# Optimization experiments

Measured on AMD Instinct MI355X. Metric: run time of the kernel, lower is better.

Reference implementation:

```python
import jax, jax.numpy as jnp
import numpy as np

B, C, H, W = 64, 3, 256, 256
K = 2  # multi_n_num
EPS_NORM = 1e-8
EPS_DEN = 1e-7
SCALE = 0.01


def setup_inputs() -> dict:
    key = jax.random.key(0)
    ka, kp, kn, kj = jax.random.split(key, 4)
    a = jax.random.normal(ka, (B, C, H, W), dtype=jnp.float32)
    p = jax.random.normal(kp, (B, C, H, W), dtype=jnp.float32)
    n = jax.random.normal(kn, (B, C, H, W), dtype=jnp.float32)
    # sample_with_j(B, 2, i) -> [i, random j != i]
    ar = jnp.arange(B, dtype=jnp.int64)
    off = jax.random.randint(kj, (B,), 1, B)  # offset in [1, B) guarantees j != i
    neg_idx = jnp.stack([ar, (ar + off) % B], axis=1).astype(jnp.int64)  # [B, K]
    return {"a": a, "p": p, "n": n, "neg_idx": neg_idx}


def _fft_norm(x):
    # torch.fft.fft2 over last two dims -> complex, same rank as x
    f = jnp.fft.fft2(x, axes=(-2, -1))  # [B, C, H, W] complex64
    # torch.norm(f, p=2, dim=1, keepdim=True) on complex = sqrt(sum |f|^2 over C)
    nrm = jnp.sqrt(jnp.sum(jnp.abs(f) ** 2, axis=1, keepdims=True))
    return f / (nrm + EPS_NORM) * SCALE


def reference(a, p, n, neg_idx):
    af = _fft_norm(a)
    pf = _fft_norm(p)
    nf = _fft_norm(n)
    # L1Loss on complex tensors = mean |diff| (complex magnitude)
    d_ap = jnp.mean(jnp.abs(af - pf), axis=(1, 2, 3))  # [B]
    n_sel = nf[neg_idx]  # [B, K, C, H, W]
    d_an = jnp.mean(jnp.abs(af[:, None] - n_sel), axis=(2, 3, 4))  # [B, K]
    contrastive = jnp.sum(d_ap[:, None] / (d_an + EPS_DEN))
    return contrastive / (K * B)
```

## Files before the change

### kernel.cpp

```cpp
#include <hip/hip_runtime.h>
#include <hip/hip_fp16.h>

#define B_ 64
#define SW_ 132
#define SIMG_ (256 * SW_)
#define TIMG_ (3 * SIMG_)
#define TELEMS_ ((size_t)B_ * TIMG_)
#define SST_ 257

__device__ __forceinline__ float2 cmul(float2 a, float2 b) {
  return make_float2(a.x * b.x - a.y * b.y, a.x * b.y + a.y * b.x);
}
__device__ __forceinline__ unsigned f2u(float2 v) {
  __half2 h = __float22half2_rn(v);
  return __builtin_bit_cast(unsigned, h);
}
__device__ __forceinline__ float2 u2f(unsigned u) {
  return __half22float2(__builtin_bit_cast(__half2, u));
}

__device__ __forceinline__ void bfly4(float2 x[4], float2 ta, float2 tb, float2 tc, bool tw) {
  float2 a = make_float2(x[0].x + x[2].x, x[0].y + x[2].y);
  float2 b = make_float2(x[0].x - x[2].x, x[0].y - x[2].y);
  float2 c = make_float2(x[1].x + x[3].x, x[1].y + x[3].y);
  float2 d = make_float2(x[1].x - x[3].x, x[1].y - x[3].y);
  float2 y1 = make_float2(b.x + d.y, b.y - d.x);
  float2 y2 = make_float2(a.x - c.x, a.y - c.y);
  float2 y3 = make_float2(b.x - d.y, b.y + d.x);
  x[0] = make_float2(a.x + c.x, a.y + c.y);
  if (tw) { y1 = cmul(y1, ta); y2 = cmul(y2, tb); y3 = cmul(y3, tc); }
  x[1] = y1; x[2] = y2; x[3] = y3;
}

__device__ __forceinline__ void swap16(unsigned& A, unsigned& B) {
  asm("v_permlane16_swap_b32 %0, %1" : "+v"(A), "+v"(B));
}
__device__ __forceinline__ void swap32(unsigned& A, unsigned& B) {
  asm("v_permlane32_swap_b32 %0, %1" : "+v"(A), "+v"(B));
}

template <int BIT>
__device__ __forceinline__ void xsel(unsigned& A, unsigned& B, int r) {
  bool hi = (r >> BIT) & 1;
  int send = hi ? (int)A : (int)B;
  int got;
  if constexpr (BIT == 0)
    got = __builtin_amdgcn_update_dpp(0, send, 0xB1, 0xF, 0xF, false);
  else if constexpr (BIT == 1)
    got = __builtin_amdgcn_update_dpp(0, send, 0x4E, 0xF, 0xF, false);
  else if constexpr (BIT == 2)
    got = __builtin_amdgcn_ds_swizzle(send, 0x101F);
  else
    got = __builtin_amdgcn_ds_swizzle(send, 0x201F);
  if (hi) A = (unsigned)got; else B = (unsigned)got;
}

__device__ __forceinline__ void xdig45(unsigned u[4]) {
  swap16(u[0], u[1]);
  swap16(u[2], u[3]);
  swap32(u[0], u[2]);
  swap32(u[1], u[3]);
}
template <int BIT>
__device__ __forceinline__ void xdig(unsigned u[4], int r) {
  xsel<BIT>(u[0], u[1], r);
  xsel<BIT>(u[2], u[3], r);
  xsel<BIT + 1>(u[0], u[2], r);
  xsel<BIT + 1>(u[1], u[3], r);
}

template <int NF>
__device__ __forceinline__ void fft256(float2 (&x)[NF][4], unsigned (&u)[NF][4],
                                       int r, const float2 tw[9]) {
#pragma unroll
  for (int f = 0; f < NF; ++f) bfly4(x[f], tw[0], tw[1], tw[2], true);
#pragma unroll
  for (int f = 0; f < NF; ++f)
#pragma unroll
    for (int s = 0; s < 4; ++s) u[f][s] = f2u(x[f][s]);
#pragma unroll
  for (int f = 0; f < NF; ++f) xdig45(u[f]);
#pragma unroll
  for (int f = 0; f < NF; ++f)
#pragma unroll
    for (int s = 0; s < 4; ++s) x[f][s] = u2f(u[f][s]);
#pragma unroll
  for (int f = 0; f < NF; ++f) bfly4(x[f], tw[3], tw[4], tw[5], true);
#pragma unroll
  for (int f = 0; f < NF; ++f)
#pragma unroll
    for (int s = 0; s < 4; ++s) u[f][s] = f2u(x[f][s]);
#pragma unroll
  for (int f = 0; f < NF; ++f) xdig<2>(u[f], r);
#pragma unroll
  for (int f = 0; f < NF; ++f)
#pragma unroll
    for (int s = 0; s < 4; ++s) x[f][s] = u2f(u[f][s]);
#pragma unroll
  for (int f = 0; f < NF; ++f) bfly4(x[f], tw[6], tw[7], tw[8], true);
#pragma unroll
  for (int f = 0; f < NF; ++f)
#pragma unroll
    for (int s = 0; s < 4; ++s) u[f][s] = f2u(x[f][s]);
#pragma unroll
  for (int f = 0; f < NF; ++f) xdig<0>(u[f], r);
#pragma unroll
  for (int f = 0; f < NF; ++f)
#pragma unroll
    for (int s = 0; s < 4; ++s) x[f][s] = u2f(u[f][s]);
#pragma unroll
  for (int f = 0; f < NF; ++f) bfly4(x[f], tw[0], tw[0], tw[0], false);
#pragma unroll
  for (int f = 0; f < NF; ++f)
#pragma unroll
    for (int s = 0; s < 4; ++s) u[f][s] = f2u(x[f][s]);
}

__global__ __launch_bounds__(1024, 4) void fft2_fused(const float* __restrict__ a,
                                                      const float* __restrict__ p,
                                                      const float* __restrict__ n,
                                                      unsigned* __restrict__ outbase) {
  __shared__ unsigned S[129 * SST_];

  int tid = threadIdx.x;
  int wv = tid >> 6;
  int r = tid & 63;
  int tensor = blockIdx.x / 192;
  int plane = blockIdx.x % 192;
  const float* in = (tensor == 0 ? a : (tensor == 1 ? p : n)) + (size_t)plane * 65536;
  unsigned* outp = outbase + (size_t)tensor * TELEMS_ + (size_t)plane * SIMG_;

  float2 tw[9];
  {
    float s, c;
    __sincosf(-6.283185307179586f * (float)r / 256.0f, &s, &c);
    tw[0] = make_float2(c, s); tw[1] = cmul(tw[0], tw[0]); tw[2] = cmul(tw[1], tw[0]);
    __sincosf(-6.283185307179586f * (float)(r & 15) / 64.0f, &s, &c);
    tw[3] = make_float2(c, s); tw[4] = cmul(tw[3], tw[3]); tw[5] = cmul(tw[4], tw[3]);
    __sincosf(-6.283185307179586f * (float)(r & 3) / 16.0f, &s, &c);
    tw[6] = make_float2(c, s); tw[7] = cmul(tw[6], tw[6]); tw[8] = cmul(tw[7], tw[6]);
  }
  int m = ((r & 3) << 4) | (((r >> 2) & 3) << 2) | (r >> 4);
  int mp = (64 - m) & 63;
  int rp = ((mp >> 4) & 3) | (((mp >> 2) & 3) << 2) | ((mp & 3) << 4);

  for (int it = 0; it < 2; ++it) {
    float2 x[4][4]; unsigned u[4][4];
#pragma unroll
    for (int f = 0; f < 4; ++f) {
      int q = it * 64 + wv + 16 * f;
      const float* rw = in + (size_t)(2 * q) * 256;
#pragma unroll
      for (int j = 0; j < 4; ++j)
        x[f][j] = make_float2(rw[r + 64 * j], rw[256 + r + 64 * j]);
    }
    fft256<4>(x, u, r, tw);
#pragma unroll
    for (int f = 0; f < 4; ++f) {
      int q = it * 64 + wv + 16 * f;
      unsigned m0 = (unsigned)__shfl((int)u[f][0], rp, 64);
      unsigned m2 = (unsigned)__shfl((int)u[f][2], rp, 64);
      unsigned m3 = (unsigned)__shfl((int)u[f][3], rp, 64);
      float2 Zk0 = u2f(u[f][0]);
      float2 Zk1 = u2f(u[f][1]);
      float2 Zm0 = u2f((m == 0) ? m0 : m3);
      float2 Zm1 = u2f((m == 0) ? m3 : m2);
      float2 Aa = make_float2(0.5f * (Zk0.x + Zm0.x), 0.5f * (Zk0.y - Zm0.y));
      float2 Ab = make_float2(0.5f * (Zk0.y + Zm0.y), 0.5f * (Zm0.x - Zk0.x));
      float2 Ba = make_float2(0.5f * (Zk1.x + Zm1.x), 0.5f * (Zk1.y - Zm1.y));
      float2 Bb = make_float2(0.5f * (Zk1.y + Zm1.y), 0.5f * (Zm1.x - Zk1.x));
      S[m * SST_ + 2 * q]          = f2u(Aa);
      S[m * SST_ + 2 * q + 1]      = f2u(Ab);
      S[(64 + m) * SST_ + 2 * q]     = f2u(Ba);
      S[(64 + m) * SST_ + 2 * q + 1] = f2u(Bb);
      if (r == 0) {
        float2 Z = u2f(u[f][2]);
        S[128 * SST_ + 2 * q]     = f2u(make_float2(Z.x, 0.0f));
        S[128 * SST_ + 2 * q + 1] = f2u(make_float2(Z.y, 0.0f));
      }
    }
  }

  __syncthreads();

  for (int it = 0; it < 2; ++it) {
    float2 x[4][4]; unsigned u[4][4];
#pragma unroll
    for (int f = 0; f < 4; ++f) {
      const unsigned* row = S + (size_t)(it * 64 + wv + 16 * f) * SST_;
#pragma unroll
      for (int j = 0; j < 4; ++j) x[f][j] = u2f(row[r + 64 * j]);
    }
    fft256<4>(x, u, r, tw);
#pragma unroll
    for (int f = 0; f < 4; ++f) {
      int c = it * 64 + wv + 16 * f;
      *(uint4*)(outp + (size_t)c * 256 + 4 * r) =
          make_uint4(u[f][0], u[f][1], u[f][2], u[f][3]);
    }
  }
  if (wv == 0) {
    float2 x1[1][4]; unsigned u1[1][4];
    const unsigned* srow = S + 128 * SST_;
#pragma unroll
    for (int j = 0; j < 4; ++j) x1[0][j] = u2f(srow[r + 64 * j]);
    fft256<1>(x1, u1, r, tw);
    *(uint4*)(outp + (size_t)128 * 256 + 4 * r) =
        make_uint4(u1[0][0], u1[0][1], u1[0][2], u1[0][3]);
  }
  if (wv >= 13) {
    int c = 129 + (wv - 13);
    *(uint4*)(outp + (size_t)c * 256 + 4 * r) = make_uint4(0, 0, 0, 0);
  }
}

__device__ __forceinline__ float cab2(float2 v) { return v.x * v.x + v.y * v.y; }

__global__ __launch_bounds__(256) void dist_kernel(const unsigned* __restrict__ af,
                                                   const unsigned* __restrict__ pf,
                                                   const unsigned* __restrict__ nf,
                                                   const int* __restrict__ neg,
                                                   float* __restrict__ acc) {
  int b = blockIdx.y;
  int j = (neg[1] == 0) ? (int)((const long long*)neg)[b * 2 + 1] : neg[b * 2 + 1];
  size_t ab = (size_t)b * TIMG_;
  size_t jb = (size_t)j * TIMG_;
  int t4 = blockIdx.x * 256 + threadIdx.x;
  int flat0 = t4 * 4;
  int k2 = flat0 >> 8;
  float w = (k2 == 0 || k2 >= 128) ? 1.0f : 2.0f;

  unsigned A[3][4], P[3][4], N[3][4], M[3][4];
#pragma unroll
  for (int ch = 0; ch < 3; ++ch) {
    uint4 t;
    t = *(const uint4*)(af + ab + ch * SIMG_ + flat0); A[ch][0]=t.x; A[ch][1]=t.y; A[ch][2]=t.z; A[ch][3]=t.w;
    t = *(const uint4*)(pf + ab + ch * SIMG_ + flat0); P[ch][0]=t.x; P[ch][1]=t.y; P[ch][2]=t.z; P[ch][3]=t.w;
    t = *(const uint4*)(nf + ab + ch * SIMG_ + flat0); N[ch][0]=t.x; N[ch][1]=t.y; N[ch][2]=t.z; N[ch][3]=t.w;
    t = *(const uint4*)(nf + jb + ch * SIMG_ + flat0); M[ch][0]=t.x; M[ch][1]=t.y; M[ch][2]=t.z; M[ch][3]=t.w;
  }
  float s_ap = 0.0f, s_a0 = 0.0f, s_a1 = 0.0f;
#pragma unroll
  for (int e = 0; e < 4; ++e) {
    float2 a0 = u2f(A[0][e]), a1 = u2f(A[1][e]), a2 = u2f(A[2][e]);
    float2 p0 = u2f(P[0][e]), p1 = u2f(P[1][e]), p2 = u2f(P[2][e]);
    float2 n0 = u2f(N[0][e]), n1 = u2f(N[1][e]), n2 = u2f(N[2][e]);
    float2 m0 = u2f(M[0][e]), m1 = u2f(M[1][e]), m2 = u2f(M[2][e]);
    float sa = 0.01f / (sqrtf(cab2(a0) + cab2(a1) + cab2(a2)) + 1e-8f);
    float sp = 0.01f / (sqrtf(cab2(p0) + cab2(p1) + cab2(p2)) + 1e-8f);
    float sn = 0.01f / (sqrtf(cab2(n0) + cab2(n1) + cab2(n2)) + 1e-8f);
    float sm = 0.01f / (sqrtf(cab2(m0) + cab2(m1) + cab2(m2)) + 1e-8f);
    float dx, dy;
    dx = a0.x * sa - p0.x * sp; dy = a0.y * sa - p0.y * sp; s_ap += sqrtf(dx * dx + dy * dy);
    dx = a1.x * sa - p1.x * sp; dy = a1.y * sa - p1.y * sp; s_ap += sqrtf(dx * dx + dy * dy);
    dx = a2.x * sa - p2.x * sp; dy = a2.y * sa - p2.y * sp; s_ap += sqrtf(dx * dx + dy * dy);
    dx = a0.x * sa - n0.x * sn; dy = a0.y * sa - n0.y * sn; s_a0 += sqrtf(dx * dx + dy * dy);
    dx = a1.x * sa - n1.x * sn; dy = a1.y * sa - n1.y * sn; s_a0 += sqrtf(dx * dx + dy * dy);
    dx = a2.x * sa - n2.x * sn; dy = a2.y * sa - n2.y * sn; s_a0 += sqrtf(dx * dx + dy * dy);
    dx = a0.x * sa - m0.x * sm; dy = a0.y * sa - m0.y * sm; s_a1 += sqrtf(dx * dx + dy * dy);
    dx = a1.x * sa - m1.x * sm; dy = a1.y * sa - m1.y * sm; s_a1 += sqrtf(dx * dx + dy * dy);
    dx = a2.x * sa - m2.x * sm; dy = a2.y * sa - m2.y * sm; s_a1 += sqrtf(dx * dx + dy * dy);
  }
  s_ap *= w; s_a0 *= w; s_a1 *= w;
#pragma unroll
  for (int off = 32; off > 0; off >>= 1) {
    s_ap += __shfl_down(s_ap, off);
    s_a0 += __shfl_down(s_a0, off);
    s_a1 += __shfl_down(s_a1, off);
  }
  __shared__ float red[3][4];
  int lane = threadIdx.x & 63, wid = threadIdx.x >> 6;
  if (lane == 0) { red[0][wid] = s_ap; red[1][wid] = s_a0; red[2][wid] = s_a1; }
  __syncthreads();
  if (threadIdx.x == 0) {
    atomicAdd(&acc[b * 3 + 0], red[0][0] + red[0][1] + red[0][2] + red[0][3]);
    atomicAdd(&acc[b * 3 + 1], red[1][0] + red[1][1] + red[1][2] + red[1][3]);
    atomicAdd(&acc[b * 3 + 2], red[2][0] + red[2][1] + red[2][2] + red[2][3]);
  }
}

__global__ void zero_acc(float* acc) { acc[threadIdx.x] = 0.0f; }

__global__ void final_kernel(const float* __restrict__ acc, float* __restrict__ out) {
  int b = threadIdx.x;
  const float inv = 1.0f / 196608.0f;
  float dap = acc[b * 3 + 0] * inv;
  float da0 = acc[b * 3 + 1] * inv;
  float da1 = acc[b * 3 + 2] * inv;
  float term = dap / (da0 + 1e-7f) + dap / (da1 + 1e-7f);
#pragma unroll
  for (int off = 32; off > 0; off >>= 1) term += __shfl_down(term, off);
  if (b == 0) out[0] = term * (1.0f / 128.0f);
}

extern "C" void kernel_launch(void* const* d_in, const int* in_sizes, int n_in,
                              void* d_out, int out_size, void* d_ws, size_t ws_size,
                              hipStream_t stream) {
  const float* a = (const float*)d_in[0];
  const float* p = (const float*)d_in[1];
  const float* n = (const float*)d_in[2];
  const int* neg = (const int*)d_in[3];
  float* out = (float*)d_out;

  unsigned* base = (unsigned*)d_ws;
  float* acc = (float*)(base + 3 * TELEMS_);

  zero_acc<<<1, 192, 0, stream>>>(acc);
  fft2_fused<<<576, 1024, 0, stream>>>(a, p, n, base);
  dist_kernel<<<dim3(33, 64), 256, 0, stream>>>(base, base + TELEMS_,
                                                base + 2 * TELEMS_, neg, acc);
  final_kernel<<<1, 64, 0, stream>>>(acc, out);
}
```

Before: 245.9 us.

## Split fused 2D FFT into row and column kernels via global intermediate

Replaces the single per-plane fused 2D FFT kernel (1024 threads, large shared-memory transpose) with two kernels. The first does the row FFTs and writes the half-spectrum to a global transposed buffer. The second does the column FFTs from small tiles staged through shared memory. The intent is more, smaller blocks for better occupancy and load balance, paid for with an extra round trip of the intermediate through global memory. The split path runs only when the workspace is large enough; otherwise the old fused path is kept.

```diff
diff --git a/kernel.cpp b/kernel.cpp
--- a/kernel.cpp
+++ b/kernel.cpp
@@ -7,6 +7,7 @@
 #define TIMG_ (3 * SIMG_)
 #define TELEMS_ ((size_t)B_ * TIMG_)
 #define SST_ 257
+#define TST_ 132
 
 __device__ __forceinline__ float2 cmul(float2 a, float2 b) {
   return make_float2(a.x * b.x - a.y * b.y, a.x * b.y + a.y * b.x);
@@ -38,7 +39,6 @@
 __device__ __forceinline__ void swap32(unsigned& A, unsigned& B) {
   asm("v_permlane32_swap_b32 %0, %1" : "+v"(A), "+v"(B));
 }
-
 template <int BIT>
 __device__ __forceinline__ void xsel(unsigned& A, unsigned& B, int r) {
   bool hi = (r >> BIT) & 1;
@@ -54,7 +54,6 @@
     got = __builtin_amdgcn_ds_swizzle(send, 0x201F);
   if (hi) A = (unsigned)got; else B = (unsigned)got;
 }
-
 __device__ __forceinline__ void xdig45(unsigned u[4]) {
   swap16(u[0], u[1]);
   swap16(u[2], u[3]);
@@ -114,6 +113,120 @@
   for (int f = 0; f < NF; ++f)
 #pragma unroll
     for (int s = 0; s < 4; ++s) u[f][s] = f2u(x[f][s]);
+}
+
+__device__ __forceinline__ void tw_init(float2 tw[9], int r) {
+  float s, c;
+  __sincosf(-6.283185307179586f * (float)r / 256.0f, &s, &c);
+  tw[0] = make_float2(c, s); tw[1] = cmul(tw[0], tw[0]); tw[2] = cmul(tw[1], tw[0]);
+  __sincosf(-6.283185307179586f * (float)(r & 15) / 64.0f, &s, &c);
+  tw[3] = make_float2(c, s); tw[4] = cmul(tw[3], tw[3]); tw[5] = cmul(tw[4], tw[3]);
+  __sincosf(-6.283185307179586f * (float)(r & 3) / 16.0f, &s, &c);
+  tw[6] = make_float2(c, s); tw[7] = cmul(tw[6], tw[6]); tw[8] = cmul(tw[7], tw[6]);
+}
+
+
+__global__ __launch_bounds__(256, 4) void fft_rows(const float* __restrict__ a,
+                                                   const float* __restrict__ p,
+                                                   const float* __restrict__ n,
+                                                   unsigned* __restrict__ T) {
+  int tid = threadIdx.x, wv = tid >> 6, r = tid & 63;
+  int plane = blockIdx.x >> 3, sub = blockIdx.x & 7;
+  int tensor = plane / 192, pl = plane % 192;
+  const float* in = (tensor == 0 ? a : (tensor == 1 ? p : n)) + (size_t)pl * 65536;
+  unsigned* Tp = T + (size_t)plane * SIMG_;
+
+  float2 tw[9];
+  tw_init(tw, r);
+  int m = ((r & 3) << 4) | (((r >> 2) & 3) << 2) | (r >> 4);
+  int mp = (64 - m) & 63;
+  int rp = ((mp >> 4) & 3) | (((mp >> 2) & 3) << 2) | ((mp & 3) << 4);
+
+  float2 x[4][4]; unsigned u[4][4];
+#pragma unroll
+  for (int f = 0; f < 4; ++f) {
+    int q = sub * 16 + wv * 4 + f;
+    const float* rw = in + (size_t)(2 * q) * 256;
+#pragma unroll
+    for (int j = 0; j < 4; ++j)
+      x[f][j] = make_float2(rw[r + 64 * j], rw[256 + r + 64 * j]);
+  }
+  fft256<4>(x, u, r, tw);
+#pragma unroll
+  for (int f = 0; f < 4; ++f) {
+    int q = sub * 16 + wv * 4 + f;
+    unsigned m0 = (unsigned)__shfl((int)u[f][0], rp, 64);
+    unsigned m2 = (unsigned)__shfl((int)u[f][2], rp, 64);
+    unsigned m3 = (unsigned)__shfl((int)u[f][3], rp, 64);
+    float2 Zk0 = u2f(u[f][0]);
+    float2 Zk1 = u2f(u[f][1]);
+    float2 Zm0 = u2f((m == 0) ? m0 : m3);
+    float2 Zm1 = u2f((m == 0) ? m3 : m2);
+    float2 Aa = make_float2(0.5f * (Zk0.x + Zm0.x), 0.5f * (Zk0.y - Zm0.y));
+    float2 Ab = make_float2(0.5f * (Zk0.y + Zm0.y), 0.5f * (Zm0.x - Zk0.x));
+    float2 Ba = make_float2(0.5f * (Zk1.x + Zm1.x), 0.5f * (Zk1.y - Zm1.y));
+    float2 Bb = make_float2(0.5f * (Zk1.y + Zm1.y), 0.5f * (Zm1.x - Zk1.x));
+    unsigned* c0 = Tp + (size_t)(2 * q) * TST_;
+    unsigned* c1 = Tp + (size_t)(2 * q + 1) * TST_;
+    c0[m]      = f2u(Aa);
+    c1[m]      = f2u(Ab);
+    c0[64 + m] = f2u(Ba);
+    c1[64 + m] = f2u(Bb);
+    if (r == 0) {
+      float2 Z = u2f(u[f][2]);
+      c0[128] = f2u(make_float2(Z.x, 0.0f));
+      c1[128] = f2u(make_float2(Z.y, 0.0f));
+    }
+  }
+}
+
+__global__ __launch_bounds__(256, 4) void fft_cols(const unsigned* __restrict__ T,
+                                                   unsigned* __restrict__ outbase) {
+  __shared__ unsigned L[256 * 17];
+  int tid = threadIdx.x, wv = tid >> 6, r = tid & 63;
+  int plane = blockIdx.x / 9, t = blockIdx.x % 9;
+  const unsigned* Tp = T + (size_t)plane * SIMG_;
+  unsigned* outp = outbase + (size_t)plane * SIMG_;
+
+  float2 tw[9];
+  tw_init(tw, r);
+
+  if (t < 8) {
+    int k0 = 16 * t;
+#pragma unroll
+    for (int i = 0; i < 16; ++i) {
+      int col = i * 16 + (tid >> 4), kk = tid & 15;
+      L[col * 17 + kk] = Tp[(size_t)col * TST_ + k0 + kk];
+    }
+    __syncthreads();
+    float2 x[4][4]; unsigned u[4][4];
+#pragma unroll
+    for (int f = 0; f < 4; ++f) {
+      int kk = wv * 4 + f;
+#pragma unroll
+      for (int j = 0; j < 4; ++j) x[f][j] = u2f(L[(r + 64 * j) * 17 + kk]);
+    }
+    fft256<4>(x, u, r, tw);
+#pragma unroll
+    for (int f = 0; f < 4; ++f) {
+      int k2 = k0 + wv * 4 + f;
+      *(uint4*)(outp + (size_t)k2 * 256 + 4 * r) =
+          make_uint4(u[f][0], u[f][1], u[f][2], u[f][3]);
+    }
+  } else {
+    if (wv == 0) {
+      float2 x1[1][4]; unsigned u1[1][4];
+#pragma unroll
+      for (int j = 0; j < 4; ++j)
+        x1[0][j] = u2f(Tp[(size_t)(r + 64 * j) * TST_ + 128]);
+      fft256<1>(x1, u1, r, tw);
+      *(uint4*)(outp + (size_t)128 * 256 + 4 * r) =
+          make_uint4(u1[0][0], u1[0][1], u1[0][2], u1[0][3]);
+    } else {
+      int c = 128 + wv;
+      *(uint4*)(outp + (size_t)c * 256 + 4 * r) = make_uint4(0, 0, 0, 0);
+    }
+  }
 }
 
 __global__ __launch_bounds__(1024, 4) void fft2_fused(const float* __restrict__ a,
@@ -131,15 +244,7 @@
   unsigned* outp = outbase + (size_t)tensor * TELEMS_ + (size_t)plane * SIMG_;
 
   float2 tw[9];
-  {
-    float s, c;
-    __sincosf(-6.283185307179586f * (float)r / 256.0f, &s, &c);
-    tw[0] = make_float2(c, s); tw[1] = cmul(tw[0], tw[0]); tw[2] = cmul(tw[1], tw[0]);
-    __sincosf(-6.283185307179586f * (float)(r & 15) / 64.0f, &s, &c);
-    tw[3] = make_float2(c, s); tw[4] = cmul(tw[3], tw[3]); tw[5] = cmul(tw[4], tw[3]);
-    __sincosf(-6.283185307179586f * (float)(r & 3) / 16.0f, &s, &c);
-    tw[6] = make_float2(c, s); tw[7] = cmul(tw[6], tw[6]); tw[8] = cmul(tw[7], tw[6]);
-  }
+  tw_init(tw, r);
   int m = ((r & 3) << 4) | (((r >> 2) & 3) << 2) | (r >> 4);
   int mp = (64 - m) & 63;
   int rp = ((mp >> 4) & 3) | (((mp >> 2) & 3) << 2) | ((mp & 3) << 4);
@@ -169,8 +274,8 @@
       float2 Ab = make_float2(0.5f * (Zk0.y + Zm0.y), 0.5f * (Zm0.x - Zk0.x));
       float2 Ba = make_float2(0.5f * (Zk1.x + Zm1.x), 0.5f * (Zk1.y - Zm1.y));
       float2 Bb = make_float2(0.5f * (Zk1.y + Zm1.y), 0.5f * (Zm1.x - Zk1.x));
-      S[m * SST_ + 2 * q]          = f2u(Aa);
-      S[m * SST_ + 2 * q + 1]      = f2u(Ab);
+      S[m * SST_ + 2 * q]            = f2u(Aa);
+      S[m * SST_ + 2 * q + 1]        = f2u(Ab);
       S[(64 + m) * SST_ + 2 * q]     = f2u(Ba);
       S[(64 + m) * SST_ + 2 * q + 1] = f2u(Bb);
       if (r == 0) {
@@ -303,11 +408,23 @@
   float* out = (float*)d_out;
 
   unsigned* base = (unsigned*)d_ws;
-  float* acc = (float*)(base + 3 * TELEMS_);
-
-  zero_acc<<<1, 192, 0, stream>>>(acc);
-  fft2_fused<<<576, 1024, 0, stream>>>(a, p, n, base);
-  dist_kernel<<<dim3(33, 64), 256, 0, stream>>>(base, base + TELEMS_,
-                                                base + 2 * TELEMS_, neg, acc);
-  final_kernel<<<1, 64, 0, stream>>>(acc, out);
-}
+  size_t need_split = (size_t)6 * TELEMS_ * 4 + 768;
+
+  if (ws_size >= need_split) {
+    unsigned* T = base + 3 * TELEMS_;
+    float* acc = (float*)(T + 3 * TELEMS_);
+    zero_acc<<<1, 192, 0, stream>>>(acc);
+    fft_rows<<<576 * 8, 256, 0, stream>>>(a, p, n, T);
+    fft_cols<<<576 * 9, 256, 0, stream>>>(T, base);
+    dist_kernel<<<dim3(33, 64), 256, 0, stream>>>(base, base + TELEMS_,
+                                                  base + 2 * TELEMS_, neg, acc);
+    final_kernel<<<1, 64, 0, stream>>>(acc, out);
+  } else {
+    float* acc = (float*)(base + 3 * TELEMS_);
+    zero_acc<<<1, 192, 0, stream>>>(acc);
+    fft2_fused<<<576, 1024, 0, stream>>>(a, p, n, base);
+    dist_kernel<<<dim3(33, 64), 256, 0, stream>>>(base, base + TELEMS_,
+                                                  base + 2 * TELEMS_, neg, acc);
+    final_kernel<<<1, 64, 0, stream>>>(acc, out);
+  }
+}
```

Measured after the change: 256.8 us. 1.04x slower.
